# Kernel tuning notes

Hardware: AMD Instinct MI355X
Metric: run time of the kernel (lower is better)

The kernel has to match this reference:

```python
import jax, jax.numpy as jnp
import numpy as np

D_MODEL = 512
NUM_HEADS = 8


def setup_inputs() -> dict:
    key = jax.random.key(0)
    ks = jax.random.split(key, 6)
    B, S, D = 4, 2048, D_MODEL
    Q = jax.random.normal(ks[0], (B, S, D), dtype=jnp.float32)
    K = jax.random.normal(ks[1], (B, S, D), dtype=jnp.float32)
    V = jax.random.normal(ks[2], (B, S, D), dtype=jnp.float32)
    # boolean mask, True = masked out; random so no row is fully masked
    mask = jax.random.randint(ks[3], (B, S, S), 0, 2).astype(jnp.bool_)
    scale = 1.0 / np.sqrt(D)
    Wq = jax.random.normal(ks[4], (D, D), dtype=jnp.float32) * scale
    Wo = jax.random.normal(ks[5], (D, D), dtype=jnp.float32) * scale
    return {"Q": Q, "K": K, "V": V, "mask": mask, "Wq": Wq, "Wo": Wo}


def reference(Q, K, V, mask, Wq, Wo):
    B, S, D = Q.shape
    H = NUM_HEADS
    dk = D // H
    # Faithful to the source: Q_Linear's weight (Wq) is applied to Q, K AND V
    # (K_Linear / V_Linear are dead parameters in the original module).
    q = (Q @ Wq.T).reshape(B, S, H, dk)
    k = (K @ Wq.T).reshape(B, S, H, dk)
    v = (V @ Wq.T).reshape(B, S, H, dk)
    # scores: [B, H, Sq, Sk]
    scores = jnp.einsum("bqhd,bkhd->bhqk", q, k)
    scores = jnp.where(mask[:, None, :, :], -jnp.inf, scores)
    w = jax.nn.softmax(scores / jnp.sqrt(jnp.asarray(dk, scores.dtype)), axis=-1)
    c = jnp.einsum("bhqk,bkhd->bqhd", w, v).reshape(B, S, D)
    return c @ Wo.T
```

## Files before the change

kernel.cpp:

```cpp
#include <hip/hip_runtime.h>
#include <math.h>

#define B_ 4
#define S_ 2048
#define D_ 512
#define H_ 8
#define DK_ 64
#define MROWS (B_ * S_)

typedef short bf16x8 __attribute__((ext_vector_type(8)));
typedef float f32x4 __attribute__((ext_vector_type(4)));

static __device__ __forceinline__ unsigned short f2bf(float x) {
    unsigned int u = __float_as_uint(x);
    return (unsigned short)((u + 0x7FFFu + ((u >> 16) & 1u)) >> 16);
}
static __device__ __forceinline__ unsigned int cvt_pk_bf16(float a, float b) {
    unsigned int r;
    asm("v_cvt_pk_bf16_f32 %0, %1, %2" : "=v"(r) : "v"(a), "v"(b));
    return r;
}
static __device__ __forceinline__ float exp2_fast(float x) {
    float r;
    asm("v_exp_f32 %0, %1" : "=v"(r) : "v"(x));
    return r;
}

#define NXE (MROWS * D_)
#define NWE (D_ * D_)
#define CAST_BLOCKS ((3 * NXE + 2 * NWE) / 8 / 256)
#define MASK_BLOCKS (B_ * S_ * S_ / 256)

__global__ __launch_bounds__(256) void prep(const float* __restrict__ Q,
                                            const float* __restrict__ K,
                                            const float* __restrict__ V,
                                            const float* __restrict__ Wq,
                                            const float* __restrict__ Wo,
                                            const void* __restrict__ mask,
                                            unsigned short* __restrict__ Qb,
                                            unsigned short* __restrict__ Kb,
                                            unsigned short* __restrict__ Vb,
                                            unsigned short* __restrict__ Wqb,
                                            unsigned short* __restrict__ Wob,
                                            unsigned long long* __restrict__ mb) {
    if (blockIdx.x < CAST_BLOCKS) {
        const int NA = NXE / 8;
        const int NWn = NWE / 8;
        int id = blockIdx.x * 256 + threadIdx.x;
        const float* src;
        unsigned short* dst;
        if (id < 3 * NA) {
            int a = id / NA, r = id - a * NA;
            src = (a == 0 ? Q : a == 1 ? K : V) + (size_t)r * 8;
            dst = (a == 0 ? Qb : a == 1 ? Kb : Vb) + (size_t)r * 8;
        } else {
            int r = id - 3 * NA;
            int a = r / NWn; r -= a * NWn;
            src = (a == 0 ? Wq : Wo) + (size_t)r * 8;
            dst = (a == 0 ? Wqb : Wob) + (size_t)r * 8;
        }
        float4 x = *(const float4*)src;
        float4 y = *(const float4*)(src + 4);
        unsigned short u[8] = {f2bf(x.x), f2bf(x.y), f2bf(x.z), f2bf(x.w),
                               f2bf(y.x), f2bf(y.y), f2bf(y.z), f2bf(y.w)};
        *(uint4*)dst = *(const uint4*)u;
    } else {
        const int id = (blockIdx.x - CAST_BLOCKS) * 256 + threadIdx.x;
        unsigned int accw = 0;
        if ((threadIdx.x & 63) == 0) {
            const unsigned int* mw0 = (const unsigned int*)mask;
            #pragma unroll
            for (int i = 0; i < 16; ++i) accw |= mw0[i];
        }
        accw = __shfl(accw, 0);
        const bool bytemode = (accw & 0xFFFFFF00u) != 0u;
        int val;
        if (bytemode) val = ((const unsigned char*)mask)[id];
        else          val = ((const int*)mask)[id];
        unsigned long long w = __ballot(val != 0);
        if ((threadIdx.x & 63) == 0) mb[id >> 6] = w;
    }
}

__global__ __launch_bounds__(256) void proj3(const unsigned short* __restrict__ Qb,
                                             const unsigned short* __restrict__ Kb,
                                             const unsigned short* __restrict__ Vb,
                                             const unsigned short* __restrict__ Wqb,
                                             unsigned short* __restrict__ qs,
                                             unsigned short* __restrict__ kbo,
                                             unsigned short* __restrict__ vt) {
    __shared__ unsigned short As[128 * 40];
    __shared__ unsigned short Bs[128 * 40];
    const int t = threadIdx.x;
    const int w = t >> 6, lane = t & 63, col = lane & 15, quad = lane >> 4;
    const int bm = blockIdx.x * 128, bn = blockIdx.y * 128;
    const int z = blockIdx.z;
    const unsigned short* X = (z == 0) ? Qb : (z == 1) ? Kb : Vb;
    const int wm = (w >> 1) * 64, wn = (w & 1) * 64;
    const int srow = t >> 1, shalf = t & 1;

    const unsigned short* xg = X + (size_t)(bm + srow) * D_ + shalf * 16;
    const unsigned short* wg = Wqb + (size_t)(bn + srow) * D_ + shalf * 16;
    unsigned short* asw = &As[srow * 40 + shalf * 16];
    unsigned short* bsw = &Bs[srow * 40 + shalf * 16];

    f32x4 acc[4][4];
    #pragma unroll
    for (int i = 0; i < 4; ++i)
        #pragma unroll
        for (int j = 0; j < 4; ++j) acc[i][j] = (f32x4){0.f, 0.f, 0.f, 0.f};

    #pragma unroll 1
    for (int k0 = 0; k0 < D_; k0 += 32) {
        __syncthreads();
        {
            uint4 a0 = *(const uint4*)(xg + k0);
            uint4 a1 = *(const uint4*)(xg + k0 + 8);
            uint4 b0 = *(const uint4*)(wg + k0);
            uint4 b1 = *(const uint4*)(wg + k0 + 8);
            *(uint4*)asw = a0; *(uint4*)(asw + 8) = a1;
            *(uint4*)bsw = b0; *(uint4*)(bsw + 8) = b1;
        }
        __syncthreads();

        bf16x8 af[4], bg[4];
        #pragma unroll
        for (int i = 0; i < 4; ++i)
            af[i] = *(const bf16x8*)&As[(wm + i * 16 + col) * 40 + quad * 8];
        #pragma unroll
        for (int j = 0; j < 4; ++j)
            bg[j] = *(const bf16x8*)&Bs[(wn + j * 16 + col) * 40 + quad * 8];
        #pragma unroll
        for (int i = 0; i < 4; ++i)
            #pragma unroll
            for (int j = 0; j < 4; ++j)
                acc[i][j] = __builtin_amdgcn_mfma_f32_16x16x32_bf16(
                    af[i], bg[j], acc[i][j], 0, 0, 0);
    }

    if (z == 2) {
        #pragma unroll
        for (int i = 0; i < 4; ++i) {
            const int R = bm + wm + i * 16 + quad * 4;
            const int bb = R >> 11, s0 = R & (S_ - 1);
            #pragma unroll
            for (int j = 0; j < 4; ++j) {
                const int C = bn + wn + j * 16 + col;
                const int hh = C >> 6, dd = C & (DK_ - 1);
                ushort4 u = make_ushort4(f2bf(acc[i][j][0]), f2bf(acc[i][j][1]),
                                         f2bf(acc[i][j][2]), f2bf(acc[i][j][3]));
                *(ushort4*)&vt[(((size_t)bb * H_ + hh) * DK_ + dd) * S_ + s0] = u;
            }
        }
    } else {
        unsigned short* O = (z == 0) ? qs : kbo;
        const float scl = (z == 0) ? 0.18033688f : 1.0f;
        #pragma unroll
        for (int i = 0; i < 4; ++i)
            #pragma unroll
            for (int j = 0; j < 4; ++j) {
                const int R = bm + wm + i * 16 + quad * 4;
                const int C = bn + wn + j * 16 + col;
                #pragma unroll
                for (int r = 0; r < 4; ++r)
                    O[(size_t)(R + r) * D_ + C] = f2bf(acc[i][j][r] * scl);
            }
    }
}

__global__ __launch_bounds__(256) void gemm_out(const unsigned short* __restrict__ Xb,
                                                const unsigned short* __restrict__ Wob,
                                                float* __restrict__ Out) {
    __shared__ unsigned short As[128 * 40];
    __shared__ unsigned short Bs[128 * 40];
    const int t = threadIdx.x;
    const int w = t >> 6, lane = t & 63, col = lane & 15, quad = lane >> 4;
    const int bm = blockIdx.x * 128, bn = blockIdx.y * 128;
    const int wm = (w >> 1) * 64, wn = (w & 1) * 64;
    const int srow = t >> 1, shalf = t & 1;

    const unsigned short* xg = Xb + (size_t)(bm + srow) * D_ + shalf * 16;
    const unsigned short* wg = Wob + (size_t)(bn + srow) * D_ + shalf * 16;
    unsigned short* asw = &As[srow * 40 + shalf * 16];
    unsigned short* bsw = &Bs[srow * 40 + shalf * 16];

    f32x4 acc[4][4];
    #pragma unroll
    for (int i = 0; i < 4; ++i)
        #pragma unroll
        for (int j = 0; j < 4; ++j) acc[i][j] = (f32x4){0.f, 0.f, 0.f, 0.f};

    #pragma unroll 1
    for (int k0 = 0; k0 < D_; k0 += 32) {
        __syncthreads();
        {
            uint4 a0 = *(const uint4*)(xg + k0);
            uint4 a1 = *(const uint4*)(xg + k0 + 8);
            uint4 b0 = *(const uint4*)(wg + k0);
            uint4 b1 = *(const uint4*)(wg + k0 + 8);
            *(uint4*)asw = a0; *(uint4*)(asw + 8) = a1;
            *(uint4*)bsw = b0; *(uint4*)(bsw + 8) = b1;
        }
        __syncthreads();

        bf16x8 af[4], bg[4];
        #pragma unroll
        for (int i = 0; i < 4; ++i)
            af[i] = *(const bf16x8*)&As[(wm + i * 16 + col) * 40 + quad * 8];
        #pragma unroll
        for (int j = 0; j < 4; ++j)
            bg[j] = *(const bf16x8*)&Bs[(wn + j * 16 + col) * 40 + quad * 8];
        #pragma unroll
        for (int i = 0; i < 4; ++i)
            #pragma unroll
            for (int j = 0; j < 4; ++j)
                acc[i][j] = __builtin_amdgcn_mfma_f32_16x16x32_bf16(
                    af[i], bg[j], acc[i][j], 0, 0, 0);
    }

    #pragma unroll
    for (int i = 0; i < 4; ++i)
        #pragma unroll
        for (int j = 0; j < 4; ++j) {
            const int R = bm + wm + i * 16 + quad * 4;
            const int C = bn + wn + j * 16 + col;
            #pragma unroll
            for (int r = 0; r < 4; ++r)
                Out[(size_t)(R + r) * D_ + C] = acc[i][j][r];
        }
}

__global__ __launch_bounds__(256) void attn_mfma(const unsigned short* __restrict__ qb,
                                                 const unsigned short* __restrict__ kb,
                                                 const unsigned short* __restrict__ vt,
                                                 const unsigned long long* __restrict__ mb,
                                                 unsigned short* __restrict__ cb) {
    __shared__ unsigned short sm[13824];
    const int t = threadIdx.x;
    const int w = t >> 6;
    const int lane = t & 63;
    const int col = lane & 15;
    const int quad = lane >> 4;
    const int h = blockIdx.y, b = blockIdx.z;
    const int bh = b * H_ + h;
    const int qrow0 = blockIdx.x * 64 + w * 16;

    const int KS = 0;
    const int VS = 4608;
    const int PS = 9216 + w * 1152;

    const unsigned int chk = cvt_pk_bf16(1.0f, 2.0f);
    const int dlo = ((chk & 0xFFFFu) == 0x3F80u) ? 0 : 16;
    const int dhi = 16 - dlo;

    const unsigned short* qrow_ptr =
        qb + (size_t)(b * S_ + qrow0 + col) * D_ + h * DK_ + quad * 8;
    bf16x8 aQ0 = *(const bf16x8*)(qrow_ptr);
    bf16x8 aQ1 = *(const bf16x8*)(qrow_ptr + 32);

    bf16x8 ones;
    #pragma unroll
    for (int i = 0; i < 8; ++i) ones[i] = (short)0x3F80;

    f32x4 O[4];
    #pragma unroll
    for (int g = 0; g < 4; ++g) O[g] = (f32x4){0.f, 0.f, 0.f, 0.f};
    f32x4 lacc = (f32x4){0.f, 0.f, 0.f, 0.f};

    const int trow = t >> 2;
    const int tseg = (t & 3) * 16;
    const unsigned short* kgp = kb + (size_t)(b * S_ + trow) * D_ + h * DK_ + tseg;
    const unsigned short* vgp = vt + ((size_t)bh * DK_ + trow) * S_ + tseg;
    unsigned short* ksw = &sm[KS + trow * 72 + tseg];
    unsigned short* vsw = &sm[VS + trow * 72 + tseg];

    const size_t mrow_base = (size_t)(b * S_ + qrow0 + quad * 4) * (S_ / 64);
    const float CREF = 8.656170245f;

    #pragma unroll 1
    for (int k0 = 0; k0 < S_; k0 += 64) {
        __syncthreads();
        {
            const unsigned short* g1 = kgp + (size_t)k0 * D_;
            uint4 a0 = *(const uint4*)g1;
            uint4 a1 = *(const uint4*)(g1 + 8);
            const unsigned short* g2 = vgp + k0;
            uint4 b0 = *(const uint4*)g2;
            uint4 b1 = *(const uint4*)(g2 + 8);
            *(uint4*)ksw = a0; *(uint4*)(ksw + 8) = a1;
            *(uint4*)vsw = b0; *(uint4*)(vsw + 8) = b1;
        }
        __syncthreads();

        unsigned long long mw[4];
        #pragma unroll
        for (int r = 0; r < 4; ++r)
            mw[r] = mb[mrow_base + (size_t)r * (S_ / 64) + (k0 >> 6)];

        f32x4 sc[4];
        #pragma unroll
        for (int g = 0; g < 4; ++g) {
            bf16x8 bk0 = *(const bf16x8*)&sm[KS + (g * 16 + col) * 72 + quad * 8];
            bf16x8 bk1 = *(const bf16x8*)&sm[KS + (g * 16 + col) * 72 + 32 + quad * 8];
            f32x4 z = {0.f, 0.f, 0.f, 0.f};
            z = __builtin_amdgcn_mfma_f32_16x16x32_bf16(aQ0, bk0, z, 0, 0, 0);
            z = __builtin_amdgcn_mfma_f32_16x16x32_bf16(aQ1, bk1, z, 0, 0, 0);
            sc[g] = z;
        }

        #pragma unroll
        for (int r = 0; r < 4; ++r) {
            const unsigned long long sh = mw[r] >> col;
            const unsigned int lo = (unsigned int)sh;
            const unsigned int hi = (unsigned int)(sh >> 32);
            float p0 = exp2_fast(((lo & 1u)       ? -1e30f : sc[0][r]) - CREF);
            float p1 = exp2_fast(((lo & 0x10000u) ? -1e30f : sc[1][r]) - CREF);
            float p2 = exp2_fast(((hi & 1u)       ? -1e30f : sc[2][r]) - CREF);
            float p3 = exp2_fast(((hi & 0x10000u) ? -1e30f : sc[3][r]) - CREF);
            const unsigned int u01 = cvt_pk_bf16(p0, p1);
            const unsigned int u23 = cvt_pk_bf16(p2, p3);
            const int prow = PS + (quad * 4 + r) * 72 + col;
            sm[prow + dlo]      = (unsigned short)u01;
            sm[prow + dhi]      = (unsigned short)(u01 >> 16);
            sm[prow + 32 + dlo] = (unsigned short)u23;
            sm[prow + 32 + dhi] = (unsigned short)(u23 >> 16);
        }
        __asm__ __volatile__("s_waitcnt lgkmcnt(0)" ::: "memory");

        bf16x8 aP0 = *(const bf16x8*)&sm[PS + col * 72 + quad * 8];
        bf16x8 aP1 = *(const bf16x8*)&sm[PS + col * 72 + 32 + quad * 8];

        lacc = __builtin_amdgcn_mfma_f32_16x16x32_bf16(aP0, ones, lacc, 0, 0, 0);
        lacc = __builtin_amdgcn_mfma_f32_16x16x32_bf16(aP1, ones, lacc, 0, 0, 0);

        #pragma unroll
        for (int g = 0; g < 4; ++g) {
            bf16x8 bv0 = *(const bf16x8*)&sm[VS + (g * 16 + col) * 72 + quad * 8];
            bf16x8 bv1 = *(const bf16x8*)&sm[VS + (g * 16 + col) * 72 + 32 + quad * 8];
            O[g] = __builtin_amdgcn_mfma_f32_16x16x32_bf16(aP0, bv0, O[g], 0, 0, 0);
            O[g] = __builtin_amdgcn_mfma_f32_16x16x32_bf16(aP1, bv1, O[g], 0, 0, 0);
        }
    }

    #pragma unroll
    for (int r = 0; r < 4; ++r) {
        const float inv = 1.0f / lacc[r];
        #pragma unroll
        for (int g = 0; g < 4; ++g)
            cb[(size_t)(b * S_ + qrow0 + quad * 4 + r) * D_ + h * DK_ + g * 16 + col] =
                f2bf(O[g][r] * inv);
    }
}

extern "C" void kernel_launch(void* const* d_in, const int* in_sizes, int n_in,
                              void* d_out, int out_size, void* d_ws, size_t ws_size,
                              hipStream_t stream) {
    const float* Q    = (const float*)d_in[0];
    const float* K    = (const float*)d_in[1];
    const float* V    = (const float*)d_in[2];
    const void*  mask = d_in[3];
    const float* Wq   = (const float*)d_in[4];
    const float* Wo   = (const float*)d_in[5];
    float* out = (float*)d_out;

    const size_t NX = (size_t)MROWS * D_;
    const size_t NW = (size_t)D_ * D_;
    unsigned short* Qb   = (unsigned short*)d_ws;
    unsigned short* Kb   = Qb + NX;
    unsigned short* Vb   = Kb + NX;
    unsigned short* Wqb  = Vb + NX;
    unsigned short* Wob  = Wqb + NW;
    unsigned short* qbuf = Wob + NW;
    unsigned short* kbuf = qbuf + NX;
    unsigned short* vtb  = kbuf + NX;
    unsigned short* cbuf = vtb + NX;
    unsigned long long* mb = (unsigned long long*)(cbuf + NX);

    prep<<<dim3(CAST_BLOCKS + MASK_BLOCKS), dim3(256), 0, stream>>>(
        Q, K, V, Wq, Wo, mask, Qb, Kb, Vb, Wqb, Wob, mb);

    proj3<<<dim3(MROWS / 128, D_ / 128, 3), dim3(256), 0, stream>>>(
        Qb, Kb, Vb, Wqb, qbuf, kbuf, vtb);

    attn_mfma<<<dim3(S_ / 64, H_, B_), dim3(256), 0, stream>>>(qbuf, kbuf, vtb, mb, cbuf);

    gemm_out<<<dim3(MROWS / 128, D_ / 128), dim3(256), 0, stream>>>(cbuf, Wob, out);
}
```

Measured before the change: 287.3 us.

## Split attention over key halves with two-row-tile waves and a combine pass

The attention kernel now splits the key range into two halves across separate blocks. Each wave handles 32 query rows instead of 16, so every K/V fragment read from shared memory feeds twice as many MFMAs. Blocks shrink to 128 threads, and the grid doubles to 256x2 blocks. Unnormalized partial outputs and row sums are written to reused workspace buffers, and a new combine kernel sums and normalizes them. This adds one kernel launch, extra global traffic, and a bf16 rounding of the partial outputs before they are summed.

Measured after the change: 337.2 us. 17.3% more time.

```diff
diff --git a/kernel.cpp b/kernel.cpp
--- a/kernel.cpp
+++ b/kernel.cpp
@@ -230,126 +230,190 @@
         }
 }
 
-__global__ __launch_bounds__(256) void attn_mfma(const unsigned short* __restrict__ qb,
+__global__ __launch_bounds__(128) void attn_mfma(const unsigned short* __restrict__ qb,
                                                  const unsigned short* __restrict__ kb,
                                                  const unsigned short* __restrict__ vt,
                                                  const unsigned long long* __restrict__ mb,
-                                                 unsigned short* __restrict__ cb) {
+                                                 unsigned short* __restrict__ o0,
+                                                 unsigned short* __restrict__ o1,
+                                                 float* __restrict__ l0,
+                                                 float* __restrict__ l1) {
     __shared__ unsigned short sm[13824];
     const int t = threadIdx.x;
     const int w = t >> 6;
     const int lane = t & 63;
     const int col = lane & 15;
     const int quad = lane >> 4;
-    const int h = blockIdx.y, b = blockIdx.z;
+    const int h = blockIdx.y;
+    const int b = blockIdx.z >> 1;
+    const int khalf = blockIdx.z & 1;
     const int bh = b * H_ + h;
-    const int qrow0 = blockIdx.x * 64 + w * 16;
+    const int qrow0 = blockIdx.x * 64 + w * 32;
+
+    unsigned short* opart = khalf ? o1 : o0;
+    float* lpart = khalf ? l1 : l0;
 
     const int KS = 0;
     const int VS = 4608;
-    const int PS = 9216 + w * 1152;
+    const int PS = 9216 + w * 2304;
 
     const unsigned int chk = cvt_pk_bf16(1.0f, 2.0f);
     const int dlo = ((chk & 0xFFFFu) == 0x3F80u) ? 0 : 16;
     const int dhi = 16 - dlo;
 
-    const unsigned short* qrow_ptr =
-        qb + (size_t)(b * S_ + qrow0 + col) * D_ + h * DK_ + quad * 8;
-    bf16x8 aQ0 = *(const bf16x8*)(qrow_ptr);
-    bf16x8 aQ1 = *(const bf16x8*)(qrow_ptr + 32);
+    bf16x8 aQ0[2], aQ1[2];
+    #pragma unroll
+    for (int s = 0; s < 2; ++s) {
+        const unsigned short* qp =
+            qb + (size_t)(b * S_ + qrow0 + s * 16 + col) * D_ + h * DK_ + quad * 8;
+        aQ0[s] = *(const bf16x8*)(qp);
+        aQ1[s] = *(const bf16x8*)(qp + 32);
+    }
 
     bf16x8 ones;
     #pragma unroll
     for (int i = 0; i < 8; ++i) ones[i] = (short)0x3F80;
 
-    f32x4 O[4];
-    #pragma unroll
-    for (int g = 0; g < 4; ++g) O[g] = (f32x4){0.f, 0.f, 0.f, 0.f};
-    f32x4 lacc = (f32x4){0.f, 0.f, 0.f, 0.f};
-
-    const int trow = t >> 2;
-    const int tseg = (t & 3) * 16;
+    f32x4 O[2][4];
+    #pragma unroll
+    for (int s = 0; s < 2; ++s)
+        #pragma unroll
+        for (int g = 0; g < 4; ++g) O[s][g] = (f32x4){0.f, 0.f, 0.f, 0.f};
+    f32x4 lacc[2];
+    lacc[0] = (f32x4){0.f, 0.f, 0.f, 0.f};
+    lacc[1] = (f32x4){0.f, 0.f, 0.f, 0.f};
+
+    const int trow = t & 63;
+    const int tseg = (t >> 6) * 32;
     const unsigned short* kgp = kb + (size_t)(b * S_ + trow) * D_ + h * DK_ + tseg;
     const unsigned short* vgp = vt + ((size_t)bh * DK_ + trow) * S_ + tseg;
     unsigned short* ksw = &sm[KS + trow * 72 + tseg];
     unsigned short* vsw = &sm[VS + trow * 72 + tseg];
 
-    const size_t mrow_base = (size_t)(b * S_ + qrow0 + quad * 4) * (S_ / 64);
     const float CREF = 8.656170245f;
+    const int kbeg = khalf * (S_ / 2);
 
     #pragma unroll 1
-    for (int k0 = 0; k0 < S_; k0 += 64) {
+    for (int k0 = kbeg; k0 < kbeg + S_ / 2; k0 += 64) {
         __syncthreads();
         {
             const unsigned short* g1 = kgp + (size_t)k0 * D_;
-            uint4 a0 = *(const uint4*)g1;
-            uint4 a1 = *(const uint4*)(g1 + 8);
+            uint4 ka0 = *(const uint4*)g1;
+            uint4 ka1 = *(const uint4*)(g1 + 8);
+            uint4 ka2 = *(const uint4*)(g1 + 16);
+            uint4 ka3 = *(const uint4*)(g1 + 24);
             const unsigned short* g2 = vgp + k0;
-            uint4 b0 = *(const uint4*)g2;
-            uint4 b1 = *(const uint4*)(g2 + 8);
-            *(uint4*)ksw = a0; *(uint4*)(ksw + 8) = a1;
-            *(uint4*)vsw = b0; *(uint4*)(vsw + 8) = b1;
-        }
-        __syncthreads();
-
-        unsigned long long mw[4];
-        #pragma unroll
-        for (int r = 0; r < 4; ++r)
-            mw[r] = mb[mrow_base + (size_t)r * (S_ / 64) + (k0 >> 6)];
-
-        f32x4 sc[4];
+            uint4 vb0 = *(const uint4*)g2;
+            uint4 vb1 = *(const uint4*)(g2 + 8);
+            uint4 vb2 = *(const uint4*)(g2 + 16);
+            uint4 vb3 = *(const uint4*)(g2 + 24);
+            *(uint4*)ksw = ka0;        *(uint4*)(ksw + 8) = ka1;
+            *(uint4*)(ksw + 16) = ka2; *(uint4*)(ksw + 24) = ka3;
+            *(uint4*)vsw = vb0;        *(uint4*)(vsw + 8) = vb1;
+            *(uint4*)(vsw + 16) = vb2; *(uint4*)(vsw + 24) = vb3;
+        }
+        __syncthreads();
+
+        f32x4 sc[2][4];
         #pragma unroll
         for (int g = 0; g < 4; ++g) {
             bf16x8 bk0 = *(const bf16x8*)&sm[KS + (g * 16 + col) * 72 + quad * 8];
             bf16x8 bk1 = *(const bf16x8*)&sm[KS + (g * 16 + col) * 72 + 32 + quad * 8];
-            f32x4 z = {0.f, 0.f, 0.f, 0.f};
-            z = __builtin_amdgcn_mfma_f32_16x16x32_bf16(aQ0, bk0, z, 0, 0, 0);
-            z = __builtin_amdgcn_mfma_f32_16x16x32_bf16(aQ1, bk1, z, 0, 0, 0);
-            sc[g] = z;
-        }
-
-        #pragma unroll
-        for (int r = 0; r < 4; ++r) {
-            const unsigned long long sh = mw[r] >> col;
-            const unsigned int lo = (unsigned int)sh;
-            const unsigned int hi = (unsigned int)(sh >> 32);
-            float p0 = exp2_fast(((lo & 1u)       ? -1e30f : sc[0][r]) - CREF);
-            float p1 = exp2_fast(((lo & 0x10000u) ? -1e30f : sc[1][r]) - CREF);
-            float p2 = exp2_fast(((hi & 1u)       ? -1e30f : sc[2][r]) - CREF);
-            float p3 = exp2_fast(((hi & 0x10000u) ? -1e30f : sc[3][r]) - CREF);
-            const unsigned int u01 = cvt_pk_bf16(p0, p1);
-            const unsigned int u23 = cvt_pk_bf16(p2, p3);
-            const int prow = PS + (quad * 4 + r) * 72 + col;
-            sm[prow + dlo]      = (unsigned short)u01;
-            sm[prow + dhi]      = (unsigned short)(u01 >> 16);
-            sm[prow + 32 + dlo] = (unsigned short)u23;
-            sm[prow + 32 + dhi] = (unsigned short)(u23 >> 16);
+            #pragma unroll
+            for (int s = 0; s < 2; ++s) {
+                f32x4 z = {0.f, 0.f, 0.f, 0.f};
+                z = __builtin_amdgcn_mfma_f32_16x16x32_bf16(aQ0[s], bk0, z, 0, 0, 0);
+                z = __builtin_amdgcn_mfma_f32_16x16x32_bf16(aQ1[s], bk1, z, 0, 0, 0);
+                sc[s][g] = z;
+            }
+        }
+
+        #pragma unroll
+        for (int s = 0; s < 2; ++s) {
+            unsigned long long mw[4];
+            #pragma unroll
+            for (int r = 0; r < 4; ++r)
+                mw[r] = mb[(size_t)(b * S_ + qrow0 + s * 16 + quad * 4 + r) * (S_ / 64)
+                           + (k0 >> 6)];
+            #pragma unroll
+            for (int r = 0; r < 4; ++r) {
+                const unsigned long long sh = mw[r] >> col;
+                const unsigned int lo = (unsigned int)sh;
+                const unsigned int hi = (unsigned int)(sh >> 32);
+                float p0 = exp2_fast(((lo & 1u)       ? -1e30f : sc[s][0][r]) - CREF);
+                float p1 = exp2_fast(((lo & 0x10000u) ? -1e30f : sc[s][1][r]) - CREF);
+                float p2 = exp2_fast(((hi & 1u)       ? -1e30f : sc[s][2][r]) - CREF);
+                float p3 = exp2_fast(((hi & 0x10000u) ? -1e30f : sc[s][3][r]) - CREF);
+                const unsigned int u01 = cvt_pk_bf16(p0, p1);
+                const unsigned int u23 = cvt_pk_bf16(p2, p3);
+                const int prow = PS + (s * 16 + quad * 4 + r) * 72 + col;
+                sm[prow + dlo]      = (unsigned short)u01;
+                sm[prow + dhi]      = (unsigned short)(u01 >> 16);
+                sm[prow + 32 + dlo] = (unsigned short)u23;
+                sm[prow + 32 + dhi] = (unsigned short)(u23 >> 16);
+            }
         }
         __asm__ __volatile__("s_waitcnt lgkmcnt(0)" ::: "memory");
 
-        bf16x8 aP0 = *(const bf16x8*)&sm[PS + col * 72 + quad * 8];
-        bf16x8 aP1 = *(const bf16x8*)&sm[PS + col * 72 + 32 + quad * 8];
-
-        lacc = __builtin_amdgcn_mfma_f32_16x16x32_bf16(aP0, ones, lacc, 0, 0, 0);
-        lacc = __builtin_amdgcn_mfma_f32_16x16x32_bf16(aP1, ones, lacc, 0, 0, 0);
+        bf16x8 aP0[2], aP1[2];
+        #pragma unroll
+        for (int s = 0; s < 2; ++s) {
+            aP0[s] = *(const bf16x8*)&sm[PS + (s * 16 + col) * 72 + quad * 8];
+            aP1[s] = *(const bf16x8*)&sm[PS + (s * 16 + col) * 72 + 32 + quad * 8];
+        }
+
+        #pragma unroll
+        for (int s = 0; s < 2; ++s) {
+            lacc[s] = __builtin_amdgcn_mfma_f32_16x16x32_bf16(aP0[s], ones, lacc[s], 0, 0, 0);
+            lacc[s] = __builtin_amdgcn_mfma_f32_16x16x32_bf16(aP1[s], ones, lacc[s], 0, 0, 0);
+        }
 
         #pragma unroll
         for (int g = 0; g < 4; ++g) {
             bf16x8 bv0 = *(const bf16x8*)&sm[VS + (g * 16 + col) * 72 + quad * 8];
             bf16x8 bv1 = *(const bf16x8*)&sm[VS + (g * 16 + col) * 72 + 32 + quad * 8];
-            O[g] = __builtin_amdgcn_mfma_f32_16x16x32_bf16(aP0, bv0, O[g], 0, 0, 0);
-            O[g] = __builtin_amdgcn_mfma_f32_16x16x32_bf16(aP1, bv1, O[g], 0, 0, 0);
-        }
-    }
-
-    #pragma unroll
-    for (int r = 0; r < 4; ++r) {
-        const float inv = 1.0f / lacc[r];
-        #pragma unroll
-        for (int g = 0; g < 4; ++g)
-            cb[(size_t)(b * S_ + qrow0 + quad * 4 + r) * D_ + h * DK_ + g * 16 + col] =
-                f2bf(O[g][r] * inv);
-    }
+            #pragma unroll
+            for (int s = 0; s < 2; ++s) {
+                O[s][g] = __builtin_amdgcn_mfma_f32_16x16x32_bf16(aP0[s], bv0, O[s][g], 0, 0, 0);
+                O[s][g] = __builtin_amdgcn_mfma_f32_16x16x32_bf16(aP1[s], bv1, O[s][g], 0, 0, 0);
+            }
+        }
+    }
+
+    #pragma unroll
+    for (int s = 0; s < 2; ++s)
+        #pragma unroll
+        for (int r = 0; r < 4; ++r) {
+            const int row = b * S_ + qrow0 + s * 16 + quad * 4 + r;
+            #pragma unroll
+            for (int g = 0; g < 4; ++g)
+                opart[(size_t)row * D_ + h * DK_ + g * 16 + col] = f2bf(O[s][g][r]);
+            if (col == 0) lpart[(size_t)row * H_ + h] = lacc[s][r];
+        }
+}
+
+__global__ __launch_bounds__(256) void combine(const unsigned short* __restrict__ o0,
+                                               const unsigned short* __restrict__ o1,
+                                               const float* __restrict__ l0,
+                                               const float* __restrict__ l1,
+                                               unsigned short* __restrict__ cb) {
+    const int id = blockIdx.x * 256 + threadIdx.x;
+    const size_t base = (size_t)id * 8;
+    const int row = (int)(base >> 9);
+    const int hh = ((int)base & (D_ - 1)) >> 6;
+    uint4 ua = *(const uint4*)(o0 + base);
+    uint4 ub = *(const uint4*)(o1 + base);
+    const float inv = 1.0f / (l0[(size_t)row * H_ + hh] + l1[(size_t)row * H_ + hh]);
+    const unsigned short* pa = (const unsigned short*)&ua;
+    const unsigned short* pb = (const unsigned short*)&ub;
+    unsigned short out[8];
+    #pragma unroll
+    for (int i = 0; i < 8; ++i) {
+        float fa = __uint_as_float((unsigned int)pa[i] << 16);
+        float fb = __uint_as_float((unsigned int)pb[i] << 16);
+        out[i] = f2bf((fa + fb) * inv);
+    }
+    *(uint4*)(cb + base) = *(const uint4*)out;
 }
 
 extern "C" void kernel_launch(void* const* d_in, const int* in_sizes, int n_in,
@@ -376,13 +440,21 @@
     unsigned short* cbuf = vtb + NX;
     unsigned long long* mb = (unsigned long long*)(cbuf + NX);
 
+    unsigned short* o0 = Qb;
+    unsigned short* o1 = Kb;
+    float* l0 = (float*)Vb;
+    float* l1 = l0 + (size_t)MROWS * H_;
+
     prep<<<dim3(CAST_BLOCKS + MASK_BLOCKS), dim3(256), 0, stream>>>(
         Q, K, V, Wq, Wo, mask, Qb, Kb, Vb, Wqb, Wob, mb);
 
     proj3<<<dim3(MROWS / 128, D_ / 128, 3), dim3(256), 0, stream>>>(
         Qb, Kb, Vb, Wqb, qbuf, kbuf, vtb);
 
-    attn_mfma<<<dim3(S_ / 64, H_, B_), dim3(256), 0, stream>>>(qbuf, kbuf, vtb, mb, cbuf);
+    attn_mfma<<<dim3(S_ / 64, H_, B_ * 2), dim3(128), 0, stream>>>(
+        qbuf, kbuf, vtb, mb, o0, o1, l0, l1);
+
+    combine<<<dim3((int)(NX / 8 / 256)), dim3(256), 0, stream>>>(o0, o1, l0, l1, cbuf);
 
     gemm_out<<<dim3(MROWS / 128, D_ / 128), dim3(256), 0, stream>>>(cbuf, Wob, out);
 }
```
